# Optimization experiments

Hardware: AMD Instinct MI355X
Metric: run time of the kernel (lower is better)

The kernel has to match this reference:

```python
import jax, jax.numpy as jnp
import numpy as np

N_NODES = 100_000
N_EDGES = 1_600_000
F_IN = 128
HID = 64
C_OUT = 16


def setup_inputs() -> dict:
    key = jax.random.key(0)
    k1, k2, k3, k4, k5 = jax.random.split(key, 5)
    x = jax.random.normal(k1, (N_NODES, F_IN), dtype=jnp.float32)
    edge_index = jax.random.randint(k2, (2, N_EDGES), 0, N_NODES, dtype=jnp.int64)
    edge_weight = jax.random.uniform(k3, (N_EDGES,), dtype=jnp.float32)
    # Glorot-ish init for the two GCNConv linear layers; PyG inits bias to zero.
    W1 = jax.random.normal(k4, (F_IN, HID), dtype=jnp.float32) * (1.0 / np.sqrt(F_IN))
    b1 = jnp.zeros((HID,), dtype=jnp.float32)
    W2 = jax.random.normal(k5, (HID, C_OUT), dtype=jnp.float32) * (1.0 / np.sqrt(HID))
    b2 = jnp.zeros((C_OUT,), dtype=jnp.float32)
    return {"x": x, "edge_index": edge_index, "edge_weight": edge_weight,
            "W1": W1, "b1": b1, "W2": W2, "b2": b2}


def gcn_layer(x, row, col, ew, W, b, n):
    """PyG GCNConv: h = D^-1/2 (A + I) D^-1/2 (x W) + b, with edge weights.
    Self loops (weight 1) are handled analytically instead of appending edges."""
    h = x @ W  # [n, out]
    deg = jax.ops.segment_sum(ew, col, num_segments=n) + 1.0  # +1 for self loop
    dinv = jax.lax.rsqrt(deg)  # deg >= 1 always
    norm = dinv[row] * ew * dinv[col]  # [E]
    agg = jax.ops.segment_sum(norm[:, None] * h[row], col, num_segments=n)
    return agg + (dinv * dinv)[:, None] * h + b


def reference(x, edge_index, edge_weight, W1, b1, W2, b2):
    row, col = edge_index[0], edge_index[1]
    h = jax.nn.relu(gcn_layer(x, row, col, edge_weight, W1, b1, N_NODES))
    # delete_min_weighted_edges(node=0): remove the min-weight edge with source 0.
    # Zeroing its weight is mathematically identical to deleting it (it then
    # contributes 0 to both the degree and the aggregation).
    masked = jnp.where(row == 0, edge_weight, jnp.inf)
    idx = jnp.argmin(masked)
    ew2 = edge_weight.at[idx].set(0.0)
    return gcn_layer(h, row, col, ew2, W2, b2, N_NODES)
```

## Files before the change

kernel.cpp:

```cpp
#include <hip/hip_runtime.h>
#include <hip/hip_bf16.h>
#include <stdint.h>

#define NN 100000
#define NE 1600000
#define FIN 128
#define HID 64
#define COUT 16

#define BUKSH 8
#define BUKN 256
#define NBUK ((NN + BUKN - 1) >> BUKSH)
#define CAP 5120
#define PART_NB 200
#define EPB (NE / PART_NB)

typedef unsigned long long u64;
typedef short bf16x8 __attribute__((ext_vector_type(8)));
typedef float f32x4 __attribute__((ext_vector_type(4)));

struct Flags { int f32; int i64; };

__device__ __forceinline__ float b2f(__hip_bfloat16 v) { return __bfloat162float(v); }

__device__ __forceinline__ float ldf(const void* p, size_t i, int f32) {
    return f32 ? ((const float*)p)[i]
               : __bfloat162float(((const __hip_bfloat16*)p)[i]);
}
__device__ __forceinline__ int lde(const void* p, size_t i, int i64) {
    return i64 ? (int)((const long long*)p)[i] : ((const int*)p)[i];
}
__device__ __forceinline__ void ld4bf(const __hip_bfloat16* p, float& x0, float& x1,
                                      float& x2, float& x3) {
    union { uint2 u; __hip_bfloat16 h[4]; } v;
    v.u = *(const uint2*)p;
    x0 = b2f(v.h[0]); x1 = b2f(v.h[1]); x2 = b2f(v.h[2]); x3 = b2f(v.h[3]);
}

__global__ void k_detect(const unsigned short* xs, const int* ei32, Flags* fl) {
    int lane = threadIdx.x & 63;
    int huge = 0;
    for (int i = lane * 2; i < 1024; i += 128) {
        int e = (xs[i] >> 7) & 0xFF;
        if (e >= 0xC0) huge = 1;
    }
    int odd_nonzero = 0;
    for (int i = 1 + lane * 2; i < 512; i += 128) {
        if (ei32[i] != 0) odd_nonzero = 1;
    }
    u64 h = __ballot(huge), o = __ballot(odd_nonzero);
    if (lane == 0) { fl->f32 = (h != 0); fl->i64 = (o == 0); }
}

__global__ void k_mink(const void* __restrict__ ei, const void* __restrict__ ew,
                       const Flags* __restrict__ fl, u64* __restrict__ minkey) {
    int e = blockIdx.x * blockDim.x + threadIdx.x;
    if (e >= NE) return;
    int r = lde(ei, e, fl->i64);
    if (r == 0) {
        float w = ldf(ew, e, fl->f32);
        u64 key = ((u64)__float_as_uint(w) << 32) | (unsigned)e;
        atomicMin(minkey, key);
    }
}

__global__ __launch_bounds__(256) void k_partA(const void* __restrict__ ei,
                                               const void* __restrict__ ew,
                                               const Flags* __restrict__ fl,
                                               const u64* __restrict__ minkey,
                                               int* __restrict__ cursorA,
                                               long long* __restrict__ tmp) {
    __shared__ int cnt[NBUK];
    __shared__ int base[NBUK];
    int b = blockIdx.x, t = threadIdx.x;
    int f32 = fl->f32, i64 = fl->i64;
    for (int i = t; i < NBUK; i += 256) cnt[i] = 0;
    __syncthreads();
    int e0 = b * EPB;
    for (int i = t; i < EPB; i += 256) {
        int c = lde(ei, (size_t)NE + e0 + i, i64);
        atomicAdd(&cnt[c >> BUKSH], 1);
    }
    __syncthreads();
    for (int i = t; i < NBUK; i += 256) {
        int n = cnt[i];
        base[i] = n ? atomicAdd(&cursorA[i], n) : 0;
    }
    __syncthreads();
    for (int i = t; i < NBUK; i += 256) cnt[i] = 0;
    __syncthreads();
    u64 k = *minkey;
    int eidx = (k == ~0ull) ? 0 : (int)(k & 0xffffffffu);
    for (int i = t; i < EPB; i += 256) {
        int e = e0 + i;
        int r = lde(ei, e, i64);
        int c = lde(ei, (size_t)NE + e, i64);
        float w = ldf(ew, e, f32);
        int buk = c >> BUKSH;
        int slot = base[buk] + atomicAdd(&cnt[buk], 1);
        if (slot < CAP) {
            unsigned lo = (unsigned)r | (((unsigned)c & 255u) << 17)
                        | ((e == eidx) ? (1u << 25) : 0u);
            tmp[(size_t)buk * CAP + slot] = ((long long)__float_as_int(w) << 32) | lo;
        }
    }
}

__global__ __launch_bounds__(512) void k_scanBk(const int* __restrict__ cursorA,
                                                int* __restrict__ bucketBase,
                                                int* __restrict__ rowptrN) {
    __shared__ int sm[512];
    int t = threadIdx.x;
    int v = 0;
    if (t < NBUK) { v = cursorA[t]; if (v > CAP) v = CAP; }
    sm[t] = v;
    for (int off = 1; off < 512; off <<= 1) {
        __syncthreads();
        int add = (t >= off) ? sm[t - off] : 0;
        __syncthreads();
        sm[t] += add;
    }
    __syncthreads();
    if (t < NBUK) bucketBase[t] = sm[t] - v;
    if (t == 511) rowptrN[NN] = sm[511];
}

__global__ __launch_bounds__(256) void k_partB(const int* __restrict__ cursorA,
                                               const int* __restrict__ bucketBase,
                                               const long long* __restrict__ tmp,
                                               int2* __restrict__ epack,
                                               int* __restrict__ rowptrN,
                                               float* __restrict__ deg,
                                               int* __restrict__ delpos) {
    __shared__ int cnt[256];
    __shared__ int pfx[256];
    __shared__ u64 wsum[256];
    int b = blockIdx.x, t = threadIdx.x;
    cnt[t] = 0; wsum[t] = 0;
    __syncthreads();
    int count = cursorA[b]; if (count > CAP) count = CAP;
    const long long* ts = tmp + (size_t)b * CAP;
    for (int i = t; i < count; i += 256) {
        long long pk = ts[i];
        unsigned lo = (unsigned)pk;
        int nl = (int)((lo >> 17) & 255u);
        atomicAdd(&cnt[nl], 1);
        float w = __int_as_float((int)(pk >> 32));
        atomicAdd(&wsum[nl], (u64)((double)w * 4294967296.0));
    }
    __syncthreads();
    int v = cnt[t];
    pfx[t] = v;
    for (int off = 1; off < 256; off <<= 1) {
        __syncthreads();
        int add = (t >= off) ? pfx[t - off] : 0;
        __syncthreads();
        pfx[t] += add;
    }
    __syncthreads();
    int excl = pfx[t] - v;
    int gbase = bucketBase[b];
    int node = (b << BUKSH) + t;
    if (node < NN) {
        rowptrN[node] = gbase + excl;
        deg[node] = (float)((double)wsum[t] * (1.0 / 4294967296.0));
    }
    __syncthreads();
    cnt[t] = gbase + excl;
    __syncthreads();
    for (int i = t; i < count; i += 256) {
        long long pk = ts[i];
        unsigned lo = (unsigned)pk;
        int nl = (int)((lo >> 17) & 255u);
        int pos = atomicAdd(&cnt[nl], 1);
        long long outpk = (pk & 0xFFFFFFFF00000000LL) | (lo & 0x1FFFFu);
        *(long long*)(epack + pos) = outpk;
        if (lo & (1u << 25)) *delpos = pos;
    }
}

__global__ void k_dinv(const float* __restrict__ deg, const void* __restrict__ ei,
                       const void* __restrict__ ew, const Flags* __restrict__ fl,
                       const u64* __restrict__ minkey,
                       float* __restrict__ dinv1, float* __restrict__ dinv2) {
    int i = blockIdx.x * blockDim.x + threadIdx.x;
    if (i >= NN) return;
    u64 k = *minkey;
    int eidx = (k == ~0ull) ? 0 : (int)(k & 0xffffffffu);
    int cmin = lde(ei, (size_t)NE + eidx, fl->i64);
    float wmin = ldf(ew, eidx, fl->f32);
    float d1 = deg[i] + 1.0f;
    float d2 = d1 - ((i == cmin) ? wmin : 0.0f);
    dinv1[i] = rsqrtf(d1);
    dinv2[i] = rsqrtf(d2);
}

__global__ __launch_bounds__(256) void k_gemm1_f32(const float* __restrict__ x,
                                                   const float* __restrict__ W1,
                                                   const Flags* __restrict__ fl,
                                                   const float* __restrict__ dinv1,
                                                   __hip_bfloat16* __restrict__ h1) {
    if (!fl->f32) return;
    __shared__ float Wp[FIN * HID];
    int t = threadIdx.x;
    int node0 = blockIdx.x * 64;
    {
        const float4* src = (const float4*)W1;
        float4* dst = (float4*)Wp;
        for (int i = t; i < 2048; i += 256) dst[i] = src[i];
    }
    __syncthreads();
    int col4 = (t & 15) * 4;
    int nb = t >> 4;
    int n0 = node0 + nb;
    const float* xr0 = x + (size_t)(n0      < NN ? n0      : NN - 1) * FIN;
    const float* xr1 = x + (size_t)(n0 + 16 < NN ? n0 + 16 : NN - 1) * FIN;
    const float* xr2 = x + (size_t)(n0 + 32 < NN ? n0 + 32 : NN - 1) * FIN;
    const float* xr3 = x + (size_t)(n0 + 48 < NN ? n0 + 48 : NN - 1) * FIN;
    float4 a0 = {0,0,0,0}, a1 = a0, a2 = a0, a3 = a0;
#pragma unroll 8
    for (int k = 0; k < FIN; k += 4) {
        float4 w0 = *(const float4*)&Wp[(k + 0) * HID + col4];
        float4 w1 = *(const float4*)&Wp[(k + 1) * HID + col4];
        float4 w2 = *(const float4*)&Wp[(k + 2) * HID + col4];
        float4 w3 = *(const float4*)&Wp[(k + 3) * HID + col4];
        float4 xv;
#define GEMM1_STEP(ACC, XR)                                              \
        xv = *(const float4*)(XR + k);                                   \
        ACC.x += xv.x * w0.x + xv.y * w1.x + xv.z * w2.x + xv.w * w3.x;  \
        ACC.y += xv.x * w0.y + xv.y * w1.y + xv.z * w2.y + xv.w * w3.y;  \
        ACC.z += xv.x * w0.z + xv.y * w1.z + xv.z * w2.z + xv.w * w3.z;  \
        ACC.w += xv.x * w0.w + xv.y * w1.w + xv.z * w2.w + xv.w * w3.w;
        GEMM1_STEP(a0, xr0)
        GEMM1_STEP(a1, xr1)
        GEMM1_STEP(a2, xr2)
        GEMM1_STEP(a3, xr3)
#undef GEMM1_STEP
    }
    float4 accs[4] = {a0, a1, a2, a3};
#pragma unroll
    for (int nn = 0; nn < 4; ++nn) {
        int node = node0 + nb + nn * 16;
        if (node < NN) {
            float dsc = dinv1[node];
            union { uint2 u; __hip_bfloat16 h[4]; } pk;
            pk.h[0] = __float2bfloat16(accs[nn].x * dsc);
            pk.h[1] = __float2bfloat16(accs[nn].y * dsc);
            pk.h[2] = __float2bfloat16(accs[nn].z * dsc);
            pk.h[3] = __float2bfloat16(accs[nn].w * dsc);
            *(uint2*)(h1 + (size_t)node * HID + col4) = pk.u;
        }
    }
}

__global__ __launch_bounds__(256) void k_gemm1_mfma(const __hip_bfloat16* __restrict__ x,
                                                    const unsigned short* __restrict__ W1,
                                                    const Flags* __restrict__ fl,
                                                    const float* __restrict__ dinv1,
                                                    __hip_bfloat16* __restrict__ h1) {
    if (fl->f32) return;
    __shared__ unsigned short Wf[8192];
    int t = threadIdx.x;
    for (int i = t; i < 8192; i += 256) {
        int k = i >> 6;
        int n = i & 63;
        int kc = k >> 5, kr = k & 31;
        int q = kr >> 3, j = kr & 7;
        int n0 = n >> 4, col = n & 15;
        Wf[((((n0 << 2) | kc) << 2) | q) * 128 + col * 8 + j] = W1[i];
    }
    __syncthreads();
    int wave = t >> 6, lane = t & 63;
    int quad = lane >> 4, col = lane & 15;
    bf16x8 B[4][4];
#pragma unroll
    for (int n0 = 0; n0 < 4; ++n0)
#pragma unroll
        for (int kc = 0; kc < 4; ++kc)
            B[kc][n0] = *(const bf16x8*)&Wf[((((n0 << 2) | kc) << 2) | quad) * 128 + col * 8];
    int tile0 = (blockIdx.x * 4 + wave) * 4;
#pragma unroll 1
    for (int i = 0; i < 4; ++i) {
        int node0 = (tile0 + i) * 16;
        if (node0 >= NN) return;
        const __hip_bfloat16* xp = x + (size_t)(node0 + col) * FIN + quad * 8;
        f32x4 a0 = {0.f, 0.f, 0.f, 0.f}, a1 = a0, a2 = a0, a3 = a0;
#pragma unroll
        for (int kc = 0; kc < 4; ++kc) {
            bf16x8 A = *(const bf16x8*)(xp + kc * 32);
            a0 = __builtin_amdgcn_mfma_f32_16x16x32_bf16(A, B[kc][0], a0, 0, 0, 0);
            a1 = __builtin_amdgcn_mfma_f32_16x16x32_bf16(A, B[kc][1], a1, 0, 0, 0);
            a2 = __builtin_amdgcn_mfma_f32_16x16x32_bf16(A, B[kc][2], a2, 0, 0, 0);
            a3 = __builtin_amdgcn_mfma_f32_16x16x32_bf16(A, B[kc][3], a3, 0, 0, 0);
        }
        __hip_bfloat16* hp = h1 + (size_t)(node0 + quad * 4) * HID + col;
#pragma unroll
        for (int r = 0; r < 4; ++r) {
            float dsc = dinv1[node0 + quad * 4 + r];
            hp[(size_t)r * HID + 0]  = __float2bfloat16(a0[r] * dsc);
            hp[(size_t)r * HID + 16] = __float2bfloat16(a1[r] * dsc);
            hp[(size_t)r * HID + 32] = __float2bfloat16(a2[r] * dsc);
            hp[(size_t)r * HID + 48] = __float2bfloat16(a3[r] * dsc);
        }
    }
}

__global__ __launch_bounds__(256) void k_agg1(const int* __restrict__ rowptrN,
                                              const int2* __restrict__ epack,
                                              const float* __restrict__ dinv1,
                                              const __hip_bfloat16* __restrict__ h1,
                                              const void* __restrict__ b1,
                                              const Flags* __restrict__ fl,
                                              float* __restrict__ out1) {
    int t = threadIdx.x;
    int n = blockIdx.x * 16 + (t >> 4);
    if (n >= NN) return;
    int l = t & 15;
    int f = l * 4;
    int wbase = t & 48;
    int f32 = fl->f32;
    float dn = dinv1[n];
    int p0 = rowptrN[n], p1 = rowptrN[n + 1];
    float a0 = 0.f, a1 = 0.f, a2 = 0.f, a3 = 0.f;
    for (int p = p0; p < p1; p += 16) {
        int idx = p + l;
        int2 ev = make_int2(0, 0);
        if (idx < p1) ev = epack[idx];
        float cw = __int_as_float(ev.y);
        int rj[16];
#pragma unroll
        for (int j = 0; j < 16; ++j)
            rj[j] = __shfl(ev.x, wbase + j);
        uint2 raw[16];
#pragma unroll
        for (int j = 0; j < 16; ++j)
            raw[j] = *(const uint2*)(h1 + (size_t)rj[j] * HID + f);
#pragma unroll
        for (int j = 0; j < 16; ++j) {
            float c = __shfl(cw, wbase + j);
            union { uint2 u; __hip_bfloat16 h[4]; } v; v.u = raw[j];
            a0 += c * b2f(v.h[0]);
            a1 += c * b2f(v.h[1]);
            a2 += c * b2f(v.h[2]);
            a3 += c * b2f(v.h[3]);
        }
    }
    float x0, x1, x2, x3;
    ld4bf(h1 + (size_t)n * HID + f, x0, x1, x2, x3);
    float4 o;
    o.x = fmaxf(dn * (a0 + x0) + ldf(b1, f + 0, f32), 0.f);
    o.y = fmaxf(dn * (a1 + x1) + ldf(b1, f + 1, f32), 0.f);
    o.z = fmaxf(dn * (a2 + x2) + ldf(b1, f + 2, f32), 0.f);
    o.w = fmaxf(dn * (a3 + x3) + ldf(b1, f + 3, f32), 0.f);
    *(float4*)(out1 + (size_t)n * HID + f) = o;
}

__global__ __launch_bounds__(256) void k_gemm2(const float* __restrict__ out1,
                                               const void* __restrict__ W2,
                                               const Flags* __restrict__ fl,
                                               const float* __restrict__ dinv2,
                                               float* __restrict__ h2) {
    __shared__ float Ws[HID * COUT];
    int t = threadIdx.x;
    int f32 = fl->f32;
    for (int i = t; i < HID * COUT; i += 256) Ws[i] = ldf(W2, i, f32);
    __syncthreads();
    int node = blockIdx.x * 64 + (t >> 2);
    if (node >= NN) return;
    int o4 = (t & 3) * 4;
    const float* xr = out1 + (size_t)node * HID;
    float a0 = 0.f, a1 = 0.f, a2 = 0.f, a3 = 0.f;
#pragma unroll 4
    for (int k = 0; k < HID; ++k) {
        float xv = xr[k];
        const float* wr = &Ws[k * COUT + o4];
        a0 += xv * wr[0]; a1 += xv * wr[1]; a2 += xv * wr[2]; a3 += xv * wr[3];
    }
    float dsc = dinv2[node];
    float* ho = h2 + (size_t)node * COUT + o4;
    ho[0] = a0 * dsc; ho[1] = a1 * dsc; ho[2] = a2 * dsc; ho[3] = a3 * dsc;
}

__global__ __launch_bounds__(256) void k_agg2(const int* __restrict__ rowptrN,
                                              const int2* __restrict__ epack,
                                              const float* __restrict__ dinv2,
                                              const float* __restrict__ h2,
                                              const void* __restrict__ bias2,
                                              const Flags* __restrict__ fl,
                                              const int* __restrict__ delpos,
                                              void* __restrict__ out) {
    int t = threadIdx.x;
    int n = blockIdx.x * 64 + (t >> 2);
    if (n >= NN) return;
    int l = t & 3;
    int f = l * 4;
    int wbase = t & 60;
    int f32 = fl->f32;
    int dp = *delpos;
    float dn = dinv2[n];
    int p0 = rowptrN[n], p1 = rowptrN[n + 1];
    float a0 = 0.f, a1 = 0.f, a2 = 0.f, a3 = 0.f;
    for (int p = p0; p < p1; p += 8) {
        int iA = p + l, iB = p + 4 + l;
        int2 evA = make_int2(0, 0), evB = make_int2(0, 0);
        if (iA < p1) evA = epack[iA];
        if (iB < p1) evB = epack[iB];
        float cwA = (iA == dp) ? 0.f : __int_as_float(evA.y);
        float cwB = (iB == dp) ? 0.f : __int_as_float(evB.y);
        int rj[8];
#pragma unroll
        for (int j = 0; j < 4; ++j) {
            rj[j]     = __shfl(evA.x, wbase + j);
            rj[4 + j] = __shfl(evB.x, wbase + j);
        }
        float4 hv[8];
#pragma unroll
        for (int j = 0; j < 8; ++j)
            hv[j] = *(const float4*)(h2 + (size_t)rj[j] * COUT + f);
#pragma unroll
        for (int j = 0; j < 4; ++j) {
            float cA = __shfl(cwA, wbase + j);
            float cB = __shfl(cwB, wbase + j);
            a0 += cA * hv[j].x + cB * hv[4 + j].x;
            a1 += cA * hv[j].y + cB * hv[4 + j].y;
            a2 += cA * hv[j].z + cB * hv[4 + j].z;
            a3 += cA * hv[j].w + cB * hv[4 + j].w;
        }
    }
    const float4 hn = *(const float4*)(h2 + (size_t)n * COUT + f);
    float o0 = dn * (a0 + hn.x) + ldf(bias2, f + 0, f32);
    float o1 = dn * (a1 + hn.y) + ldf(bias2, f + 1, f32);
    float o2 = dn * (a2 + hn.z) + ldf(bias2, f + 2, f32);
    float o3 = dn * (a3 + hn.w) + ldf(bias2, f + 3, f32);
    size_t idx = (size_t)n * COUT + f;
    if (f32) {
        float* op = (float*)out + idx;
        op[0] = o0; op[1] = o1; op[2] = o2; op[3] = o3;
    } else {
        union { uint2 u; __hip_bfloat16 h[4]; } pk;
        pk.h[0] = __float2bfloat16(o0); pk.h[1] = __float2bfloat16(o1);
        pk.h[2] = __float2bfloat16(o2); pk.h[3] = __float2bfloat16(o3);
        *(uint2*)((__hip_bfloat16*)out + idx) = pk.u;
    }
}

extern "C" void kernel_launch(void* const* d_in, const int* in_sizes, int n_in,
                              void* d_out, int out_size, void* d_ws, size_t ws_size,
                              hipStream_t stream) {
    const void* x  = d_in[0];
    const void* ei = d_in[1];
    const void* ew = d_in[2];
    const void* W1 = d_in[3];
    const void* b1 = d_in[4];
    const void* W2 = d_in[5];
    const void* b2 = d_in[6];

    char* wsb = (char*)d_ws;
    float* dinv1    = (float*)wsb;                     wsb += (size_t)NN * 4;
    float* dinv2    = (float*)wsb;                     wsb += (size_t)NN * 4;
    float* deg      = (float*)wsb;                     wsb += (size_t)NN * 4;
    int*   rowptrN  = (int*)wsb;                       wsb += (size_t)(NN + 1) * 4;
    int*   cursorA  = (int*)wsb;                       wsb += (size_t)NBUK * 4;
    int*   bucketBase = (int*)wsb;                     wsb += (size_t)NBUK * 4;
    wsb = (char*)(((uintptr_t)wsb + 15) & ~(uintptr_t)15);
    int2*  epack    = (int2*)wsb;                      wsb += (size_t)NE * 8;
    __hip_bfloat16* h1 = (__hip_bfloat16*)wsb;         wsb += (size_t)NN * HID * 2;
    float* h2       = (float*)wsb;                     wsb += (size_t)NN * COUT * 4;
    long long* tmp  = (long long*)wsb;
    float* out1     = (float*)wsb;                     wsb += (size_t)NN * HID * 4;
    u64*   minkey   = (u64*)wsb;                       wsb += 8;
    Flags* fl       = (Flags*)wsb;                     wsb += 8;
    int*   delpos   = (int*)wsb;                       wsb += 8;

    hipMemsetAsync(cursorA, 0, (size_t)NBUK * 4, stream);
    hipMemsetAsync(minkey, 0xFF, 8, stream);
    hipMemsetAsync(delpos, 0xFF, 4, stream);

    k_detect<<<1, 64, 0, stream>>>((const unsigned short*)x, (const int*)ei, fl);
    k_mink<<<(NE + 255) / 256, 256, 0, stream>>>(ei, ew, fl, minkey);
    k_partA<<<PART_NB, 256, 0, stream>>>(ei, ew, fl, minkey, cursorA, tmp);
    k_scanBk<<<1, 512, 0, stream>>>(cursorA, bucketBase, rowptrN);
    k_partB<<<NBUK, 256, 0, stream>>>(cursorA, bucketBase, tmp, epack, rowptrN,
                                      deg, delpos);
    k_dinv<<<(NN + 255) / 256, 256, 0, stream>>>(deg, ei, ew, fl, minkey, dinv1, dinv2);
    k_gemm1_f32<<<(NN + 63) / 64, 256, 0, stream>>>((const float*)x, (const float*)W1,
                                                    fl, dinv1, h1);
    k_gemm1_mfma<<<(NN / 16 + 15) / 16, 256, 0, stream>>>((const __hip_bfloat16*)x,
                                                          (const unsigned short*)W1, fl,
                                                          dinv1, h1);
    k_agg1<<<(NN + 15) / 16, 256, 0, stream>>>(rowptrN, epack, dinv1, h1, b1, fl, out1);
    k_gemm2<<<(NN + 63) / 64, 256, 0, stream>>>(out1, W2, fl, dinv2, h2);
    k_agg2<<<(NN + 63) / 64, 256, 0, stream>>>(rowptrN, epack, dinv2, h2, b2, fl,
                                               delpos, d_out);
}
```

Before: 289.3 us.

## Split hidden features into two bf16 planes and aggregate each half separately

Stores the layer-1 transformed features as two column halves (32 features each) and runs the layer-1 gather aggregation twice, once per half, so each random gather pass touches a smaller working set of about 6.4MB that is more likely to stay cache resident. It also folds the degree-to-dinv computation into the partition kernel, which removes one kernel launch and the deg buffer. The trade-off is that the CSR edge list and row pointers are now read twice, and each gather fetches only 64 bytes per neighbor row.

```diff
diff --git a/kernel.cpp b/kernel.cpp
--- a/kernel.cpp
+++ b/kernel.cpp
@@ -130,7 +130,12 @@
                                                const long long* __restrict__ tmp,
                                                int2* __restrict__ epack,
                                                int* __restrict__ rowptrN,
-                                               float* __restrict__ deg,
+                                               const void* __restrict__ ei,
+                                               const void* __restrict__ ew,
+                                               const Flags* __restrict__ fl,
+                                               const u64* __restrict__ minkey,
+                                               float* __restrict__ dinv1,
+                                               float* __restrict__ dinv2,
                                                int* __restrict__ delpos) {
     __shared__ int cnt[256];
     __shared__ int pfx[256];
@@ -163,7 +168,15 @@
     int node = (b << BUKSH) + t;
     if (node < NN) {
         rowptrN[node] = gbase + excl;
-        deg[node] = (float)((double)wsum[t] * (1.0 / 4294967296.0));
+        float degv = (float)((double)wsum[t] * (1.0 / 4294967296.0));
+        u64 kk = *minkey;
+        int eidx = (kk == ~0ull) ? 0 : (int)(kk & 0xffffffffu);
+        int cmin = lde(ei, (size_t)NE + eidx, fl->i64);
+        float wmin = ldf(ew, eidx, fl->f32);
+        float d1 = degv + 1.0f;
+        float d2 = d1 - ((node == cmin) ? wmin : 0.0f);
+        dinv1[node] = rsqrtf(d1);
+        dinv2[node] = rsqrtf(d2);
     }
     __syncthreads();
     cnt[t] = gbase + excl;
@@ -179,27 +192,12 @@
     }
 }
 
-__global__ void k_dinv(const float* __restrict__ deg, const void* __restrict__ ei,
-                       const void* __restrict__ ew, const Flags* __restrict__ fl,
-                       const u64* __restrict__ minkey,
-                       float* __restrict__ dinv1, float* __restrict__ dinv2) {
-    int i = blockIdx.x * blockDim.x + threadIdx.x;
-    if (i >= NN) return;
-    u64 k = *minkey;
-    int eidx = (k == ~0ull) ? 0 : (int)(k & 0xffffffffu);
-    int cmin = lde(ei, (size_t)NE + eidx, fl->i64);
-    float wmin = ldf(ew, eidx, fl->f32);
-    float d1 = deg[i] + 1.0f;
-    float d2 = d1 - ((i == cmin) ? wmin : 0.0f);
-    dinv1[i] = rsqrtf(d1);
-    dinv2[i] = rsqrtf(d2);
-}
-
 __global__ __launch_bounds__(256) void k_gemm1_f32(const float* __restrict__ x,
                                                    const float* __restrict__ W1,
                                                    const Flags* __restrict__ fl,
                                                    const float* __restrict__ dinv1,
-                                                   __hip_bfloat16* __restrict__ h1) {
+                                                   __hip_bfloat16* __restrict__ h1a,
+                                                   __hip_bfloat16* __restrict__ h1b) {
     if (!fl->f32) return;
     __shared__ float Wp[FIN * HID];
     int t = threadIdx.x;
@@ -237,6 +235,8 @@
         GEMM1_STEP(a3, xr3)
 #undef GEMM1_STEP
     }
+    __hip_bfloat16* plane = (col4 >= 32) ? h1b : h1a;
+    int c = col4 & 31;
     float4 accs[4] = {a0, a1, a2, a3};
 #pragma unroll
     for (int nn = 0; nn < 4; ++nn) {
@@ -248,7 +248,7 @@
             pk.h[1] = __float2bfloat16(accs[nn].y * dsc);
             pk.h[2] = __float2bfloat16(accs[nn].z * dsc);
             pk.h[3] = __float2bfloat16(accs[nn].w * dsc);
-            *(uint2*)(h1 + (size_t)node * HID + col4) = pk.u;
+            *(uint2*)(plane + (size_t)node * 32 + c) = pk.u;
         }
     }
 }
@@ -257,7 +257,8 @@
                                                     const unsigned short* __restrict__ W1,
                                                     const Flags* __restrict__ fl,
                                                     const float* __restrict__ dinv1,
-                                                    __hip_bfloat16* __restrict__ h1) {
+                                                    __hip_bfloat16* __restrict__ h1a,
+                                                    __hip_bfloat16* __restrict__ h1b) {
     if (fl->f32) return;
     __shared__ unsigned short Wf[8192];
     int t = threadIdx.x;
@@ -293,50 +294,52 @@
             a2 = __builtin_amdgcn_mfma_f32_16x16x32_bf16(A, B[kc][2], a2, 0, 0, 0);
             a3 = __builtin_amdgcn_mfma_f32_16x16x32_bf16(A, B[kc][3], a3, 0, 0, 0);
         }
-        __hip_bfloat16* hp = h1 + (size_t)(node0 + quad * 4) * HID + col;
+        __hip_bfloat16* pa = h1a + (size_t)(node0 + quad * 4) * 32 + col;
+        __hip_bfloat16* pb = h1b + (size_t)(node0 + quad * 4) * 32 + col;
 #pragma unroll
         for (int r = 0; r < 4; ++r) {
             float dsc = dinv1[node0 + quad * 4 + r];
-            hp[(size_t)r * HID + 0]  = __float2bfloat16(a0[r] * dsc);
-            hp[(size_t)r * HID + 16] = __float2bfloat16(a1[r] * dsc);
-            hp[(size_t)r * HID + 32] = __float2bfloat16(a2[r] * dsc);
-            hp[(size_t)r * HID + 48] = __float2bfloat16(a3[r] * dsc);
-        }
-    }
-}
-
-__global__ __launch_bounds__(256) void k_agg1(const int* __restrict__ rowptrN,
-                                              const int2* __restrict__ epack,
-                                              const float* __restrict__ dinv1,
-                                              const __hip_bfloat16* __restrict__ h1,
-                                              const void* __restrict__ b1,
-                                              const Flags* __restrict__ fl,
-                                              float* __restrict__ out1) {
+            pa[(size_t)r * 32 + 0]  = __float2bfloat16(a0[r] * dsc);
+            pa[(size_t)r * 32 + 16] = __float2bfloat16(a1[r] * dsc);
+            pb[(size_t)r * 32 + 0]  = __float2bfloat16(a2[r] * dsc);
+            pb[(size_t)r * 32 + 16] = __float2bfloat16(a3[r] * dsc);
+        }
+    }
+}
+
+__global__ __launch_bounds__(256) void k_agg1h(const int* __restrict__ rowptrN,
+                                               const int2* __restrict__ epack,
+                                               const float* __restrict__ dinv1,
+                                               const __hip_bfloat16* __restrict__ plane,
+                                               const void* __restrict__ b1,
+                                               const Flags* __restrict__ fl,
+                                               float* __restrict__ out1,
+                                               int halfOff) {
     int t = threadIdx.x;
-    int n = blockIdx.x * 16 + (t >> 4);
+    int n = blockIdx.x * 32 + (t >> 3);
     if (n >= NN) return;
-    int l = t & 15;
+    int l = t & 7;
     int f = l * 4;
-    int wbase = t & 48;
+    int wbase = t & 56;
     int f32 = fl->f32;
     float dn = dinv1[n];
     int p0 = rowptrN[n], p1 = rowptrN[n + 1];
     float a0 = 0.f, a1 = 0.f, a2 = 0.f, a3 = 0.f;
-    for (int p = p0; p < p1; p += 16) {
+    for (int p = p0; p < p1; p += 8) {
         int idx = p + l;
         int2 ev = make_int2(0, 0);
         if (idx < p1) ev = epack[idx];
         float cw = __int_as_float(ev.y);
-        int rj[16];
-#pragma unroll
-        for (int j = 0; j < 16; ++j)
+        int rj[8];
+#pragma unroll
+        for (int j = 0; j < 8; ++j)
             rj[j] = __shfl(ev.x, wbase + j);
-        uint2 raw[16];
-#pragma unroll
-        for (int j = 0; j < 16; ++j)
-            raw[j] = *(const uint2*)(h1 + (size_t)rj[j] * HID + f);
-#pragma unroll
-        for (int j = 0; j < 16; ++j) {
+        uint2 raw[8];
+#pragma unroll
+        for (int j = 0; j < 8; ++j)
+            raw[j] = *(const uint2*)(plane + (size_t)rj[j] * 32 + f);
+#pragma unroll
+        for (int j = 0; j < 8; ++j) {
             float c = __shfl(cw, wbase + j);
             union { uint2 u; __hip_bfloat16 h[4]; } v; v.u = raw[j];
             a0 += c * b2f(v.h[0]);
@@ -346,13 +349,13 @@
         }
     }
     float x0, x1, x2, x3;
-    ld4bf(h1 + (size_t)n * HID + f, x0, x1, x2, x3);
+    ld4bf(plane + (size_t)n * 32 + f, x0, x1, x2, x3);
     float4 o;
-    o.x = fmaxf(dn * (a0 + x0) + ldf(b1, f + 0, f32), 0.f);
-    o.y = fmaxf(dn * (a1 + x1) + ldf(b1, f + 1, f32), 0.f);
-    o.z = fmaxf(dn * (a2 + x2) + ldf(b1, f + 2, f32), 0.f);
-    o.w = fmaxf(dn * (a3 + x3) + ldf(b1, f + 3, f32), 0.f);
-    *(float4*)(out1 + (size_t)n * HID + f) = o;
+    o.x = fmaxf(dn * (a0 + x0) + ldf(b1, halfOff + f + 0, f32), 0.f);
+    o.y = fmaxf(dn * (a1 + x1) + ldf(b1, halfOff + f + 1, f32), 0.f);
+    o.z = fmaxf(dn * (a2 + x2) + ldf(b1, halfOff + f + 2, f32), 0.f);
+    o.w = fmaxf(dn * (a3 + x3) + ldf(b1, halfOff + f + 3, f32), 0.f);
+    *(float4*)(out1 + (size_t)n * HID + halfOff + f) = o;
 }
 
 __global__ __launch_bounds__(256) void k_gemm2(const float* __restrict__ out1,
@@ -458,13 +461,13 @@
     char* wsb = (char*)d_ws;
     float* dinv1    = (float*)wsb;                     wsb += (size_t)NN * 4;
     float* dinv2    = (float*)wsb;                     wsb += (size_t)NN * 4;
-    float* deg      = (float*)wsb;                     wsb += (size_t)NN * 4;
     int*   rowptrN  = (int*)wsb;                       wsb += (size_t)(NN + 1) * 4;
     int*   cursorA  = (int*)wsb;                       wsb += (size_t)NBUK * 4;
     int*   bucketBase = (int*)wsb;                     wsb += (size_t)NBUK * 4;
     wsb = (char*)(((uintptr_t)wsb + 15) & ~(uintptr_t)15);
     int2*  epack    = (int2*)wsb;                      wsb += (size_t)NE * 8;
-    __hip_bfloat16* h1 = (__hip_bfloat16*)wsb;         wsb += (size_t)NN * HID * 2;
+    __hip_bfloat16* h1a = (__hip_bfloat16*)wsb;        wsb += (size_t)NN * 32 * 2;
+    __hip_bfloat16* h1b = (__hip_bfloat16*)wsb;        wsb += (size_t)NN * 32 * 2;
     float* h2       = (float*)wsb;                     wsb += (size_t)NN * COUT * 4;
     long long* tmp  = (long long*)wsb;
     float* out1     = (float*)wsb;                     wsb += (size_t)NN * HID * 4;
@@ -481,14 +484,16 @@
     k_partA<<<PART_NB, 256, 0, stream>>>(ei, ew, fl, minkey, cursorA, tmp);
     k_scanBk<<<1, 512, 0, stream>>>(cursorA, bucketBase, rowptrN);
     k_partB<<<NBUK, 256, 0, stream>>>(cursorA, bucketBase, tmp, epack, rowptrN,
-                                      deg, delpos);
-    k_dinv<<<(NN + 255) / 256, 256, 0, stream>>>(deg, ei, ew, fl, minkey, dinv1, dinv2);
+                                      ei, ew, fl, minkey, dinv1, dinv2, delpos);
     k_gemm1_f32<<<(NN + 63) / 64, 256, 0, stream>>>((const float*)x, (const float*)W1,
-                                                    fl, dinv1, h1);
+                                                    fl, dinv1, h1a, h1b);
     k_gemm1_mfma<<<(NN / 16 + 15) / 16, 256, 0, stream>>>((const __hip_bfloat16*)x,
                                                           (const unsigned short*)W1, fl,
-                                                          dinv1, h1);
-    k_agg1<<<(NN + 15) / 16, 256, 0, stream>>>(rowptrN, epack, dinv1, h1, b1, fl, out1);
+                                                          dinv1, h1a, h1b);
+    k_agg1h<<<(NN + 31) / 32, 256, 0, stream>>>(rowptrN, epack, dinv1, h1a, b1, fl,
+                                                out1, 0);
+    k_agg1h<<<(NN + 31) / 32, 256, 0, stream>>>(rowptrN, epack, dinv1, h1b, b1, fl,
+                                                out1, 32);
     k_gemm2<<<(NN + 63) / 64, 256, 0, stream>>>(out1, W2, fl, dinv2, h2);
     k_agg2<<<(NN + 63) / 64, 256, 0, stream>>>(rowptrN, epack, dinv2, h2, b2, fl,
                                                delpos, d_out);
```

Result: slower. 298.8 us (+3.3%).

## Use split-bf16 MFMA for fp32 GEMM1 and fuse dinv into partition kernel

Applied to the files above, without the earlier changes.

Replaces the scalar fp32 FMA first-layer GEMM with an MFMA kernel that splits x and W1 into bf16 hi/lo parts and accumulates three bf16 products to approximate fp32 accuracy. It also folds the degree-to-rsqrt computation into k_partB, removing the separate k_dinv launch and the deg buffer round trip. The split-bf16 scheme trades extra MFMA work and conversion ALU for matrix-core throughput, with a small precision loss from dropping the lo*lo term.

```diff
diff --git a/kernel.cpp b/kernel.cpp
--- a/kernel.cpp
+++ b/kernel.cpp
@@ -35,6 +35,16 @@
     union { uint2 u; __hip_bfloat16 h[4]; } v;
     v.u = *(const uint2*)p;
     x0 = b2f(v.h[0]); x1 = b2f(v.h[1]); x2 = b2f(v.h[2]); x3 = b2f(v.h[3]);
+}
+__device__ __forceinline__ unsigned short f2bfu(float f) {
+    union { __hip_bfloat16 b; unsigned short u; } c;
+    c.b = __float2bfloat16(f);
+    return c.u;
+}
+__device__ __forceinline__ float bfu2f(unsigned short u) {
+    union { unsigned short h[2]; float f; } c;
+    c.h[0] = 0; c.h[1] = u;
+    return c.f;
 }
 
 __global__ void k_detect(const unsigned short* xs, const int* ei32, Flags* fl) {
@@ -130,7 +140,12 @@
                                                const long long* __restrict__ tmp,
                                                int2* __restrict__ epack,
                                                int* __restrict__ rowptrN,
-                                               float* __restrict__ deg,
+                                               const void* __restrict__ ei,
+                                               const void* __restrict__ ew,
+                                               const Flags* __restrict__ fl,
+                                               const u64* __restrict__ minkey,
+                                               float* __restrict__ dinv1,
+                                               float* __restrict__ dinv2,
                                                int* __restrict__ delpos) {
     __shared__ int cnt[256];
     __shared__ int pfx[256];
@@ -163,7 +178,15 @@
     int node = (b << BUKSH) + t;
     if (node < NN) {
         rowptrN[node] = gbase + excl;
-        deg[node] = (float)((double)wsum[t] * (1.0 / 4294967296.0));
+        float degv = (float)((double)wsum[t] * (1.0 / 4294967296.0));
+        u64 kk = *minkey;
+        int eidx = (kk == ~0ull) ? 0 : (int)(kk & 0xffffffffu);
+        int cmin = lde(ei, (size_t)NE + eidx, fl->i64);
+        float wmin = ldf(ew, eidx, fl->f32);
+        float d1 = degv + 1.0f;
+        float d2 = d1 - ((node == cmin) ? wmin : 0.0f);
+        dinv1[node] = rsqrtf(d1);
+        dinv2[node] = rsqrtf(d2);
     }
     __syncthreads();
     cnt[t] = gbase + excl;
@@ -179,76 +202,90 @@
     }
 }
 
-__global__ void k_dinv(const float* __restrict__ deg, const void* __restrict__ ei,
-                       const void* __restrict__ ew, const Flags* __restrict__ fl,
-                       const u64* __restrict__ minkey,
-                       float* __restrict__ dinv1, float* __restrict__ dinv2) {
-    int i = blockIdx.x * blockDim.x + threadIdx.x;
-    if (i >= NN) return;
-    u64 k = *minkey;
-    int eidx = (k == ~0ull) ? 0 : (int)(k & 0xffffffffu);
-    int cmin = lde(ei, (size_t)NE + eidx, fl->i64);
-    float wmin = ldf(ew, eidx, fl->f32);
-    float d1 = deg[i] + 1.0f;
-    float d2 = d1 - ((i == cmin) ? wmin : 0.0f);
-    dinv1[i] = rsqrtf(d1);
-    dinv2[i] = rsqrtf(d2);
-}
-
-__global__ __launch_bounds__(256) void k_gemm1_f32(const float* __restrict__ x,
-                                                   const float* __restrict__ W1,
-                                                   const Flags* __restrict__ fl,
-                                                   const float* __restrict__ dinv1,
-                                                   __hip_bfloat16* __restrict__ h1) {
+__global__ __launch_bounds__(256, 3) void k_gemm1_split(const float* __restrict__ x,
+                                                        const float* __restrict__ W1,
+                                                        const Flags* __restrict__ fl,
+                                                        const float* __restrict__ dinv1,
+                                                        __hip_bfloat16* __restrict__ h1) {
     if (!fl->f32) return;
-    __shared__ float Wp[FIN * HID];
+    __shared__ __align__(16) unsigned short Whi[8192];
+    __shared__ __align__(16) unsigned short Wlo[8192];
     int t = threadIdx.x;
-    int node0 = blockIdx.x * 64;
-    {
-        const float4* src = (const float4*)W1;
-        float4* dst = (float4*)Wp;
-        for (int i = t; i < 2048; i += 256) dst[i] = src[i];
-    }
-    __syncthreads();
-    int col4 = (t & 15) * 4;
-    int nb = t >> 4;
-    int n0 = node0 + nb;
-    const float* xr0 = x + (size_t)(n0      < NN ? n0      : NN - 1) * FIN;
-    const float* xr1 = x + (size_t)(n0 + 16 < NN ? n0 + 16 : NN - 1) * FIN;
-    const float* xr2 = x + (size_t)(n0 + 32 < NN ? n0 + 32 : NN - 1) * FIN;
-    const float* xr3 = x + (size_t)(n0 + 48 < NN ? n0 + 48 : NN - 1) * FIN;
-    float4 a0 = {0,0,0,0}, a1 = a0, a2 = a0, a3 = a0;
-#pragma unroll 8
-    for (int k = 0; k < FIN; k += 4) {
-        float4 w0 = *(const float4*)&Wp[(k + 0) * HID + col4];
-        float4 w1 = *(const float4*)&Wp[(k + 1) * HID + col4];
-        float4 w2 = *(const float4*)&Wp[(k + 2) * HID + col4];
-        float4 w3 = *(const float4*)&Wp[(k + 3) * HID + col4];
-        float4 xv;
-#define GEMM1_STEP(ACC, XR)                                              \
-        xv = *(const float4*)(XR + k);                                   \
-        ACC.x += xv.x * w0.x + xv.y * w1.x + xv.z * w2.x + xv.w * w3.x;  \
-        ACC.y += xv.x * w0.y + xv.y * w1.y + xv.z * w2.y + xv.w * w3.y;  \
-        ACC.z += xv.x * w0.z + xv.y * w1.z + xv.z * w2.z + xv.w * w3.z;  \
-        ACC.w += xv.x * w0.w + xv.y * w1.w + xv.z * w2.w + xv.w * w3.w;
-        GEMM1_STEP(a0, xr0)
-        GEMM1_STEP(a1, xr1)
-        GEMM1_STEP(a2, xr2)
-        GEMM1_STEP(a3, xr3)
-#undef GEMM1_STEP
-    }
-    float4 accs[4] = {a0, a1, a2, a3};
-#pragma unroll
-    for (int nn = 0; nn < 4; ++nn) {
-        int node = node0 + nb + nn * 16;
-        if (node < NN) {
-            float dsc = dinv1[node];
-            union { uint2 u; __hip_bfloat16 h[4]; } pk;
-            pk.h[0] = __float2bfloat16(accs[nn].x * dsc);
-            pk.h[1] = __float2bfloat16(accs[nn].y * dsc);
-            pk.h[2] = __float2bfloat16(accs[nn].z * dsc);
-            pk.h[3] = __float2bfloat16(accs[nn].w * dsc);
-            *(uint2*)(h1 + (size_t)node * HID + col4) = pk.u;
+    for (int i = t; i < 8192; i += 256) {
+        int k = i >> 6;
+        int n = i & 63;
+        int kc = k >> 5, kr = k & 31;
+        int q = kr >> 3, j = kr & 7;
+        int n0 = n >> 4, col = n & 15;
+        float w = W1[i];
+        unsigned short hi = f2bfu(w);
+        unsigned short lo = f2bfu(w - bfu2f(hi));
+        int idx = ((n0 << 4) + (kc << 2) + q) * 128 + col * 8 + j;
+        Whi[idx] = hi;
+        Wlo[idx] = lo;
+    }
+    __syncthreads();
+    int wave = t >> 6, lane = t & 63;
+    int quad = lane >> 4, col = lane & 15;
+    bf16x8 Bh[4][4];
+#pragma unroll
+    for (int n0 = 0; n0 < 4; ++n0)
+#pragma unroll
+        for (int kc = 0; kc < 4; ++kc)
+            Bh[kc][n0] = *(const bf16x8*)&Whi[((n0 << 4) + (kc << 2) + quad) * 128 + col * 8];
+    int tile0 = (blockIdx.x * 4 + wave) * 2;
+#pragma unroll 1
+    for (int i = 0; i < 2; ++i) {
+        int node0 = (tile0 + i) * 16;
+        if (node0 >= NN) return;
+        const float* xp = x + (size_t)(node0 + col) * FIN + quad * 8;
+        float4 xv[8];
+#pragma unroll
+        for (int kc = 0; kc < 4; ++kc) {
+            xv[2 * kc]     = *(const float4*)(xp + kc * 32);
+            xv[2 * kc + 1] = *(const float4*)(xp + kc * 32 + 4);
+        }
+        f32x4 a0 = {0.f, 0.f, 0.f, 0.f}, a1 = a0, a2 = a0, a3 = a0;
+#pragma unroll
+        for (int kc = 0; kc < 4; ++kc) {
+            float fv[8];
+            fv[0] = xv[2 * kc].x;     fv[1] = xv[2 * kc].y;
+            fv[2] = xv[2 * kc].z;     fv[3] = xv[2 * kc].w;
+            fv[4] = xv[2 * kc + 1].x; fv[5] = xv[2 * kc + 1].y;
+            fv[6] = xv[2 * kc + 1].z; fv[7] = xv[2 * kc + 1].w;
+            bf16x8 Ah, Al;
+#pragma unroll
+            for (int j = 0; j < 8; ++j) {
+                unsigned short hi = f2bfu(fv[j]);
+                Ah[j] = (short)hi;
+                Al[j] = (short)f2bfu(fv[j] - bfu2f(hi));
+            }
+            int lbase = ((kc << 2) + quad) * 128 + col * 8;
+            bf16x8 Bl0 = *(const bf16x8*)&Wlo[lbase];
+            bf16x8 Bl1 = *(const bf16x8*)&Wlo[(1 << 4) * 128 + lbase];
+            bf16x8 Bl2 = *(const bf16x8*)&Wlo[(2 << 4) * 128 + lbase];
+            bf16x8 Bl3 = *(const bf16x8*)&Wlo[(3 << 4) * 128 + lbase];
+            a0 = __builtin_amdgcn_mfma_f32_16x16x32_bf16(Ah, Bh[kc][0], a0, 0, 0, 0);
+            a0 = __builtin_amdgcn_mfma_f32_16x16x32_bf16(Al, Bh[kc][0], a0, 0, 0, 0);
+            a0 = __builtin_amdgcn_mfma_f32_16x16x32_bf16(Ah, Bl0,      a0, 0, 0, 0);
+            a1 = __builtin_amdgcn_mfma_f32_16x16x32_bf16(Ah, Bh[kc][1], a1, 0, 0, 0);
+            a1 = __builtin_amdgcn_mfma_f32_16x16x32_bf16(Al, Bh[kc][1], a1, 0, 0, 0);
+            a1 = __builtin_amdgcn_mfma_f32_16x16x32_bf16(Ah, Bl1,      a1, 0, 0, 0);
+            a2 = __builtin_amdgcn_mfma_f32_16x16x32_bf16(Ah, Bh[kc][2], a2, 0, 0, 0);
+            a2 = __builtin_amdgcn_mfma_f32_16x16x32_bf16(Al, Bh[kc][2], a2, 0, 0, 0);
+            a2 = __builtin_amdgcn_mfma_f32_16x16x32_bf16(Ah, Bl2,      a2, 0, 0, 0);
+            a3 = __builtin_amdgcn_mfma_f32_16x16x32_bf16(Ah, Bh[kc][3], a3, 0, 0, 0);
+            a3 = __builtin_amdgcn_mfma_f32_16x16x32_bf16(Al, Bh[kc][3], a3, 0, 0, 0);
+            a3 = __builtin_amdgcn_mfma_f32_16x16x32_bf16(Ah, Bl3,      a3, 0, 0, 0);
+        }
+        __hip_bfloat16* hp = h1 + (size_t)(node0 + quad * 4) * HID + col;
+#pragma unroll
+        for (int r = 0; r < 4; ++r) {
+            float dsc = dinv1[node0 + quad * 4 + r];
+            hp[(size_t)r * HID + 0]  = __float2bfloat16(a0[r] * dsc);
+            hp[(size_t)r * HID + 16] = __float2bfloat16(a1[r] * dsc);
+            hp[(size_t)r * HID + 32] = __float2bfloat16(a2[r] * dsc);
+            hp[(size_t)r * HID + 48] = __float2bfloat16(a3[r] * dsc);
         }
     }
 }
@@ -259,7 +296,7 @@
                                                     const float* __restrict__ dinv1,
                                                     __hip_bfloat16* __restrict__ h1) {
     if (fl->f32) return;
-    __shared__ unsigned short Wf[8192];
+    __shared__ __align__(16) unsigned short Wf[8192];
     int t = threadIdx.x;
     for (int i = t; i < 8192; i += 256) {
         int k = i >> 6;
@@ -458,7 +495,6 @@
     char* wsb = (char*)d_ws;
     float* dinv1    = (float*)wsb;                     wsb += (size_t)NN * 4;
     float* dinv2    = (float*)wsb;                     wsb += (size_t)NN * 4;
-    float* deg      = (float*)wsb;                     wsb += (size_t)NN * 4;
     int*   rowptrN  = (int*)wsb;                       wsb += (size_t)(NN + 1) * 4;
     int*   cursorA  = (int*)wsb;                       wsb += (size_t)NBUK * 4;
     int*   bucketBase = (int*)wsb;                     wsb += (size_t)NBUK * 4;
@@ -481,10 +517,10 @@
     k_partA<<<PART_NB, 256, 0, stream>>>(ei, ew, fl, minkey, cursorA, tmp);
     k_scanBk<<<1, 512, 0, stream>>>(cursorA, bucketBase, rowptrN);
     k_partB<<<NBUK, 256, 0, stream>>>(cursorA, bucketBase, tmp, epack, rowptrN,
-                                      deg, delpos);
-    k_dinv<<<(NN + 255) / 256, 256, 0, stream>>>(deg, ei, ew, fl, minkey, dinv1, dinv2);
-    k_gemm1_f32<<<(NN + 63) / 64, 256, 0, stream>>>((const float*)x, (const float*)W1,
-                                                    fl, dinv1, h1);
+                                      ei, ew, fl, minkey, dinv1, dinv2, delpos);
+    k_gemm1_split<<<(NN / 16 + 7) / 8, 256, 0, stream>>>((const float*)x,
+                                                         (const float*)W1, fl,
+                                                         dinv1, h1);
     k_gemm1_mfma<<<(NN / 16 + 15) / 16, 256, 0, stream>>>((const __hip_bfloat16*)x,
                                                           (const unsigned short*)W1, fl,
                                                           dinv1, h1);
```

Result: faster. 276.2 us (-4.5%).
